# Optimization experiments

Measured on AMD Instinct MI355X. Metric: run time of the kernel, lower is better.

## Reference

```python
import jax, jax.numpy as jnp
import numpy as np

B, S, D, H, DFF = 2, 2048, 1024, 16, 4096
DK = D // H
EPS = 1e-6


def layer_norm(x, alpha, bias):
    # TF reduce_std is biased std; eps added to std (not variance)
    mean = jnp.mean(x, axis=-1, keepdims=True)
    std = jnp.sqrt(jnp.mean((x - mean) ** 2, axis=-1, keepdims=True))
    return alpha * (x - mean) / (std + EPS) + bias


def setup_inputs() -> dict:
    key = jax.random.key(0)
    ks = jax.random.split(key, 10)
    s = 0.02
    return {
        "x": jax.random.normal(ks[0], (B, S, D), jnp.float32),
        "mask": jnp.ones((B, 1, 1, S), jnp.int32),
        "wq": jax.random.normal(ks[1], (D, D), jnp.float32) * s,
        "wk": jax.random.normal(ks[2], (D, D), jnp.float32) * s,
        "wv": jax.random.normal(ks[3], (D, D), jnp.float32) * s,
        "wo": jax.random.normal(ks[4], (D, D), jnp.float32) * s,
        "w1": jax.random.normal(ks[5], (D, DFF), jnp.float32) * s,
        "b1": jnp.zeros((DFF,), jnp.float32),
        "w2": jax.random.normal(ks[6], (DFF, D), jnp.float32) * s,
        "b2": jnp.zeros((D,), jnp.float32),
        "ln1_a": jnp.ones((D,), jnp.float32),
        "ln1_b": jnp.zeros((D,), jnp.float32),
        "ln2_a": jnp.ones((D,), jnp.float32),
        "ln2_b": jnp.zeros((D,), jnp.float32),
    }


def reference(x, mask, wq, wk, wv, wo, w1, b1, w2, b2, ln1_a, ln1_b, ln2_a, ln2_b):
    # --- residual 1: pre-norm self-attention ---
    xn = layer_norm(x, ln1_a, ln1_b)
    q = (xn @ wq).reshape(B, S, H, DK)
    k = (xn @ wk).reshape(B, S, H, DK)
    v = (xn @ wv).reshape(B, S, H, DK)
    scores = jnp.einsum('bqhd,bkhd->bhqk', q, k) / jnp.sqrt(jnp.float32(DK))
    scores = jnp.where(mask == 0, jnp.float32(-1e9), scores)
    attn = jax.nn.softmax(scores, axis=-1)  # dropout = identity at eval
    ctx = jnp.einsum('bhqk,bkhd->bqhd', attn, v).reshape(B, S, D)
    x = x + ctx @ wo
    # --- residual 2: pre-norm FFN ---
    xn = layer_norm(x, ln2_a, ln2_b)
    ff = jax.nn.relu(xn @ w1 + b1) @ w2 + b2
    return x + ff
```

## Files before the change

kernel.cpp:

```cpp
#include <hip/hip_runtime.h>

#define BATCH 2
#define SEQ   2048
#define DMODEL 1024
#define NHEAD 16
#define DHEAD 64
#define DFF_  4096
#define MROWS (BATCH*SEQ)
#define EPS 1e-6f

typedef unsigned short u16;
typedef unsigned int u32;
typedef __bf16 bf16x8 __attribute__((ext_vector_type(8)));
typedef float  f32x4  __attribute__((ext_vector_type(4)));
typedef u32    u32x2  __attribute__((ext_vector_type(2)));

__device__ __forceinline__ float bf2f(u16 h) {
    union { u32 u; float f; } v; v.u = ((u32)h) << 16; return v.f;
}
__device__ __forceinline__ u16 f2bf(float f) {
    union { float f; u32 u; } v; v.f = f;
    u32 u = v.u;
    u32 r = (u + 0x7fffu + ((u >> 16) & 1u)) >> 16;
    return (u16)r;
}

__device__ __forceinline__ void async16(const u16* g, u16* l) {
    __builtin_amdgcn_global_load_lds((const __attribute__((address_space(1))) void*)g,
                                     (__attribute__((address_space(3))) void*)l,
                                     16, 0, 0);
}

__global__ __launch_bounds__(256) void transpose_cvt(const float* __restrict__ in,
                                                     u16* __restrict__ out,
                                                     int R, int C) {
    __shared__ float tile[32][33];
    int c0 = blockIdx.x * 32, r0 = blockIdx.y * 32;
    int x = threadIdx.x, y = threadIdx.y;
    #pragma unroll
    for (int i = 0; i < 32; i += 8)
        tile[y + i][x] = in[(size_t)(r0 + y + i) * C + c0 + x];
    __syncthreads();
    #pragma unroll
    for (int i = 0; i < 32; i += 8)
        out[(size_t)(c0 + y + i) * R + r0 + x] = f2bf(tile[x][y + i]);
}

__global__ __launch_bounds__(256) void transpose_cvt4(const float* __restrict__ i0,
                                                      const float* __restrict__ i1,
                                                      const float* __restrict__ i2,
                                                      const float* __restrict__ i3,
                                                      u16* __restrict__ o0,
                                                      u16* __restrict__ o1,
                                                      u16* __restrict__ o2,
                                                      u16* __restrict__ o3) {
    __shared__ float tile[32][33];
    const float* in; u16* out;
    switch (blockIdx.z) {
        case 0: in = i0; out = o0; break;
        case 1: in = i1; out = o1; break;
        case 2: in = i2; out = o2; break;
        default: in = i3; out = o3; break;
    }
    int c0 = blockIdx.x * 32, r0 = blockIdx.y * 32;
    int x = threadIdx.x, y = threadIdx.y;
    #pragma unroll
    for (int i = 0; i < 32; i += 8)
        tile[y + i][x] = in[(size_t)(r0 + y + i) * DMODEL + c0 + x];
    __syncthreads();
    #pragma unroll
    for (int i = 0; i < 32; i += 8)
        out[(size_t)(c0 + y + i) * DMODEL + r0 + x] = f2bf(tile[x][y + i]);
}

__global__ __launch_bounds__(256) void transpose_v_perm(const u16* __restrict__ qkv,
                                                        u16* __restrict__ vtp) {
    __shared__ u16 tile[64][72];
    int kt = blockIdx.x * 64;
    int bh = blockIdx.y; int b = bh >> 4, h = bh & 15;
    const u16* in = qkv + ((size_t)(b * SEQ + kt)) * 3072 + 2 * DMODEL + h * DHEAD;
    u16* out = vtp + ((size_t)bh * DHEAD) * SEQ;
    int t = threadIdx.x;
    int r = t >> 3, c8 = (t & 7) * 8;
    #pragma unroll
    for (int pass = 0; pass < 2; pass++) {
        int row = r + pass * 32;
        uint4 v = *(const uint4*)(in + (size_t)row * 3072 + c8);
        *(uint4*)&tile[row][c8] = v;
    }
    __syncthreads();
    #pragma unroll
    for (int pass = 0; pass < 2; pass++) {
        int d = r + pass * 32;
        u16 o8[8];
        #pragma unroll
        for (int e = 0; e < 8; e++) {
            int c = c8 + e;
            o8[e] = tile[(c & 3) * 16 + (c >> 2)][d];
        }
        *(uint4*)(out + (size_t)d * SEQ + kt + c8) = *(const uint4*)o8;
    }
}

__global__ __launch_bounds__(256) void ln_kernel(const float* __restrict__ x,
                                                 const float* __restrict__ alpha,
                                                 const float* __restrict__ beta,
                                                 u16* __restrict__ out) {
    int row = blockIdx.x;
    int t = threadIdx.x;
    const float* xr = x + (size_t)row * DMODEL;
    float4 xv = ((const float4*)xr)[t];
    float f0 = xv.x, f1 = xv.y, f2 = xv.z, f3 = xv.w;
    float s1 = f0 + f1 + f2 + f3;
    float s2 = f0*f0 + f1*f1 + f2*f2 + f3*f3;
    #pragma unroll
    for (int off = 32; off >= 1; off >>= 1) {
        s1 += __shfl_xor(s1, off);
        s2 += __shfl_xor(s2, off);
    }
    __shared__ float r1[4], r2[4];
    int w = t >> 6, lane = t & 63;
    if (lane == 0) { r1[w] = s1; r2[w] = s2; }
    __syncthreads();
    s1 = r1[0] + r1[1] + r1[2] + r1[3];
    s2 = r2[0] + r2[1] + r2[2] + r2[3];
    float mean = s1 * (1.0f / DMODEL);
    float var  = s2 * (1.0f / DMODEL) - mean * mean;
    var = fmaxf(var, 0.0f);
    float inv = 1.0f / (sqrtf(var) + EPS);
    float4 av = ((const float4*)alpha)[t];
    float4 bv = ((const float4*)beta)[t];
    ushort4 ov;
    ov.x = f2bf(av.x * (f0 - mean) * inv + bv.x);
    ov.y = f2bf(av.y * (f1 - mean) * inv + bv.y);
    ov.z = f2bf(av.z * (f2 - mean) * inv + bv.z);
    ov.w = f2bf(av.w * (f3 - mean) * inv + bv.w);
    ((ushort4*)(out + (size_t)row * DMODEL))[t] = ov;
}

#define BK 64

template <int AI, int AJ, bool OUT_F32>
__global__ __launch_bounds__(256) void gemm_bt(const u16* __restrict__ A,
                                               const u16* __restrict__ BT,
                                               void* __restrict__ Cp,
                                               const float* __restrict__ bias,
                                               const float* __restrict__ residual,
                                               int M, int N, int K, int do_relu) {
    constexpr int BMt = AI * 32, BNt = AJ * 32;
    __shared__ u16 As[BMt * BK];
    __shared__ u16 Bs[BNt * BK];
    int t = threadIdx.x;
    int bx = blockIdx.x;
    if ((gridDim.x & 7) == 0) {
        int cpx = gridDim.x >> 3;
        bx = (bx & 7) * cpx + (bx >> 3);
    }
    int m0 = blockIdx.y * BMt, n0 = bx * BNt;
    int lane = t & 63, w = t >> 6;
    int wr = w >> 1, wc = w & 1;
    int lhi = lane >> 4, llo = lane & 15;
    int sr = lane >> 3, sk = lane & 7;
    int skx = (sk ^ sr) * 8;

    f32x4 acc[AI][AJ] = {};

    const u16* Ab = A  + (size_t)m0 * K + skx;
    const u16* Bb = BT + (size_t)n0 * K + skx;

    for (int k0 = 0; k0 < K; k0 += BK) {
        __syncthreads();
        #pragma unroll
        for (int j = 0; j < AI; j++) {
            int blk = w * AI + j;
            async16(Ab + (size_t)(blk * 8 + sr) * K + k0, &As[blk * 512]);
        }
        #pragma unroll
        for (int j = 0; j < AJ; j++) {
            int blk = w * AJ + j;
            async16(Bb + (size_t)(blk * 8 + sr) * K + k0, &Bs[blk * 512]);
        }
        __syncthreads();
        #pragma unroll
        for (int kk = 0; kk < 2; kk++) {
            int slot = ((kk * 4 + lhi) ^ (llo & 7)) * 8;
            bf16x8 af[AI], bfr[AJ];
            #pragma unroll
            for (int i = 0; i < AI; i++)
                af[i]  = *(const bf16x8*)(&As[(wr * 16 * AI + i * 16 + llo) * 64 + slot]);
            #pragma unroll
            for (int j = 0; j < AJ; j++)
                bfr[j] = *(const bf16x8*)(&Bs[(wc * 16 * AJ + j * 16 + llo) * 64 + slot]);
            #pragma unroll
            for (int i = 0; i < AI; i++)
                #pragma unroll
                for (int j = 0; j < AJ; j++)
                    acc[i][j] = __builtin_amdgcn_mfma_f32_16x16x32_bf16(af[i], bfr[j], acc[i][j], 0, 0, 0);
        }
    }

    #pragma unroll
    for (int i = 0; i < AI; i++) {
        #pragma unroll
        for (int rr = 0; rr < 4; rr++) {
            int row = m0 + wr * 16 * AI + i * 16 + lhi * 4 + rr;
            #pragma unroll
            for (int j = 0; j < AJ; j++) {
                int col = n0 + wc * 16 * AJ + j * 16 + llo;
                float v = acc[i][j][rr];
                if (bias)      v += bias[col];
                if (residual)  v += residual[(size_t)row * N + col];
                if (do_relu)   v = fmaxf(v, 0.0f);
                size_t idx = (size_t)row * N + col;
                if (OUT_F32) ((float*)Cp)[idx] = v;
                else         ((u16*)Cp)[idx]   = f2bf(v);
            }
        }
    }
}

#define SCL 0.18033688f

__global__ __launch_bounds__(256) void flash_attn(const u16* __restrict__ qkv,
                                                  const u16* __restrict__ vtp,
                                                  const int* __restrict__ mask,
                                                  u16* __restrict__ ctx) {
    __shared__ u16 QPs[64 * 64];
    __shared__ u16 Ks[64 * 64];
    __shared__ u16 VTs[64 * 64];
    __shared__ float mbias[64];

    int t = threadIdx.x;
    int w = t >> 6, lane = t & 63, lhi = lane >> 4, llo = lane & 15;
    int sr = lane >> 3, sk = lane & 7;
    int skx = (sk ^ sr) * 8;

    int f  = (blockIdx.z * NHEAD + blockIdx.y) * (SEQ / 64) + blockIdx.x;
    int s  = f & 31;
    int q0 = (f >> 5) * 64;
    int hb = (s & 7) * 4 + (s >> 3);
    int h = hb & 15, b = hb >> 4;

    const u16* Qg  = qkv + ((size_t)(b * SEQ + q0)) * 3072 + h * DHEAD;
    const u16* Kg  = qkv + ((size_t)(b * SEQ)) * 3072 + DMODEL + h * DHEAD;
    const u16* VTg = vtp + ((size_t)((b * NHEAD + h) * DHEAD)) * SEQ;

    #pragma unroll
    for (int j = 0; j < 2; j++) {
        int blk = w * 2 + j;
        async16(Qg + (size_t)(blk * 8 + sr) * 3072 + skx, &QPs[blk * 512]);
    }
    __syncthreads();
    bf16x8 qf[2];
    #pragma unroll
    for (int kk = 0; kk < 2; kk++)
        qf[kk] = *(const bf16x8*)&QPs[(w * 16 + llo) * 64 + ((kk * 4 + lhi) ^ (llo & 7)) * 8];

    u16* Ps = QPs + w * 1024;

    float l_part[4] = {};
    f32x4 o_acc[4] = {};

    for (int kt = 0; kt < SEQ; kt += 64) {
        __syncthreads();
        #pragma unroll
        for (int j = 0; j < 2; j++) {
            int blk = w * 2 + j;
            async16(Kg  + (size_t)(kt + blk * 8 + sr) * 3072 + skx, &Ks[blk * 512]);
            async16(VTg + (size_t)(blk * 8 + sr) * SEQ + kt + skx,  &VTs[blk * 512]);
        }
        if (t < 64) mbias[t] = (mask[b * SEQ + kt + t] == 0) ? -1.0e12f : 0.0f;
        __syncthreads();

        f32x4 s4[4] = {};
        #pragma unroll
        for (int kk = 0; kk < 2; kk++) {
            #pragma unroll
            for (int j = 0; j < 4; j++) {
                bf16x8 kf = *(const bf16x8*)&Ks[(j * 16 + llo) * 64 +
                                                ((kk * 4 + lhi) ^ (llo & 7)) * 8];
                s4[j] = __builtin_amdgcn_mfma_f32_16x16x32_bf16(qf[kk], kf, s4[j], 0, 0, 0);
            }
        }
        float mb[4];
        #pragma unroll
        for (int j = 0; j < 4; j++) mb[j] = mbias[j * 16 + llo];

        #pragma unroll
        for (int rr = 0; rr < 4; rr++) {
            u32 pu[4];
            #pragma unroll
            for (int j = 0; j < 4; j++) {
                float p = __builtin_amdgcn_exp2f(__builtin_fmaf(s4[j][rr], SCL, mb[j]));
                l_part[rr] += p;
                union { float f; u32 u; } c; c.f = p;
                pu[j] = c.u;
            }
            u32x2 pw;
            pw[0] = (pu[0] >> 16) | (pu[1] & 0xffff0000u);
            pw[1] = (pu[2] >> 16) | (pu[3] & 0xffff0000u);
            int prow = lhi * 4 + rr;
            *(u32x2*)&Ps[prow * 64 + ((llo >> 1) ^ (prow & 7)) * 8 + (llo & 1) * 4] = pw;
        }
        #pragma unroll
        for (int kk = 0; kk < 2; kk++) {
            bf16x8 pf = *(const bf16x8*)&Ps[llo * 64 + ((kk * 4 + lhi) ^ (llo & 7)) * 8];
            #pragma unroll
            for (int nb = 0; nb < 4; nb++) {
                bf16x8 vf = *(const bf16x8*)&VTs[(nb * 16 + llo) * 64 +
                                                 ((kk * 4 + lhi) ^ (llo & 7)) * 8];
                o_acc[nb] = __builtin_amdgcn_mfma_f32_16x16x32_bf16(pf, vf, o_acc[nb], 0, 0, 0);
            }
        }
    }

    #pragma unroll
    for (int rr = 0; rr < 4; rr++) {
        float l = l_part[rr];
        #pragma unroll
        for (int off = 1; off <= 8; off <<= 1) l += __shfl_xor(l, off);
        float inv = __builtin_amdgcn_rcpf(l);
        int row = q0 + w * 16 + lhi * 4 + rr;
        #pragma unroll
        for (int nb = 0; nb < 4; nb++) {
            int col = h * DHEAD + nb * 16 + llo;
            ctx[((size_t)(b * SEQ) + row) * DMODEL + col] = f2bf(o_acc[nb][rr] * inv);
        }
    }
}

extern "C" void kernel_launch(void* const* d_in, const int* in_sizes, int n_in,
                              void* d_out, int out_size, void* d_ws, size_t ws_size,
                              hipStream_t stream) {
    (void)in_sizes; (void)n_in; (void)out_size; (void)ws_size;
    const float* x    = (const float*)d_in[0];
    const int* mask   = (const int*)d_in[1];
    const float* wq   = (const float*)d_in[2];
    const float* wk   = (const float*)d_in[3];
    const float* wv   = (const float*)d_in[4];
    const float* wo   = (const float*)d_in[5];
    const float* w1   = (const float*)d_in[6];
    const float* b1   = (const float*)d_in[7];
    const float* w2   = (const float*)d_in[8];
    const float* b2   = (const float*)d_in[9];
    const float* ln1a = (const float*)d_in[10];
    const float* ln1b = (const float*)d_in[11];
    const float* ln2a = (const float*)d_in[12];
    const float* ln2b = (const float*)d_in[13];
    float* out = (float*)d_out;

    char* wsb = (char*)d_ws;
    const size_t MB = 1024 * 1024;
    u16*   wqkvT = (u16*)(wsb + 0);
    u16*   woT   = (u16*)(wsb + 6 * MB);
    u16*   w1T   = (u16*)(wsb + 8 * MB);
    u16*   w2T   = (u16*)(wsb + 16 * MB);
    u16*   xn    = (u16*)(wsb + 24 * MB);
    float* x2    = (float*)(wsb + 32 * MB);
    u16*   vtp   = (u16*)(wsb + 32 * MB);
    u16*   ctx   = (u16*)(wsb + 48 * MB);
    u16*   qkv   = (u16*)(wsb + 56 * MB);
    u16*   ff1   = (u16*)(wsb + 56 * MB);

    dim3 tb(32, 8);
    transpose_cvt4<<<dim3(DMODEL/32, DMODEL/32, 4), tb, 0, stream>>>(
        wq, wk, wv, wo,
        wqkvT, wqkvT + 1024*1024, wqkvT + 2*1024*1024, woT);
    transpose_cvt<<<dim3(DFF_/32,  DMODEL/32),  tb, 0, stream>>>(w1, w1T, DMODEL, DFF_);
    transpose_cvt<<<dim3(DMODEL/32, DFF_/32),   tb, 0, stream>>>(w2, w2T, DFF_, DMODEL);

    ln_kernel<<<MROWS, 256, 0, stream>>>(x, ln1a, ln1b, xn);
    gemm_bt<4,2,false><<<dim3(3072/64, MROWS/128), 256, 0, stream>>>(xn, wqkvT, qkv,
                                                                     nullptr, nullptr,
                                                                     MROWS, 3072, DMODEL, 0);
    transpose_v_perm<<<dim3(SEQ/64, BATCH*NHEAD), 256, 0, stream>>>(qkv, vtp);
    flash_attn<<<dim3(SEQ/64, NHEAD, BATCH), 256, 0, stream>>>(qkv, vtp, mask, ctx);
    gemm_bt<2,2,true><<<dim3(DMODEL/64, MROWS/64), 256, 0, stream>>>(ctx, woT, x2,
                                                                     nullptr, x,
                                                                     MROWS, DMODEL, DMODEL, 0);
    ln_kernel<<<MROWS, 256, 0, stream>>>(x2, ln2a, ln2b, xn);
    gemm_bt<4,2,false><<<dim3(DFF_/64, MROWS/128), 256, 0, stream>>>(xn, w1T, ff1,
                                                                    b1, nullptr,
                                                                    MROWS, DFF_, DMODEL, 1);
    gemm_bt<2,2,true><<<dim3(DMODEL/64, MROWS/64), 256, 0, stream>>>(ff1, w2T, out,
                                                                    b2, x2,
                                                                    MROWS, DMODEL, DFF_, 0);
}
```

Measured before the change: 372.3 us.

## Split-K the FFN down-projection with atomic accumulation into LN-initialized output

The final FFN down-projection GEMM (K=4096) is split into two K halves along a new grid z dimension, and each half atomically adds its partial into the fp32 output. The second layernorm kernel now pre-initializes the output with residual plus b2, so the GEMM epilogue no longer adds bias or residual. The aim is to double the block count of this long-K GEMM for better CU occupancy. The cost is atomic traffic, an extra full fp32 write in the layernorm, and nondeterministic summation order.

```diff
diff --git a/kernel.cpp b/kernel.cpp
--- a/kernel.cpp
+++ b/kernel.cpp
@@ -105,7 +105,9 @@
 __global__ __launch_bounds__(256) void ln_kernel(const float* __restrict__ x,
                                                  const float* __restrict__ alpha,
                                                  const float* __restrict__ beta,
-                                                 u16* __restrict__ out) {
+                                                 u16* __restrict__ out,
+                                                 const float* __restrict__ abias,
+                                                 float* __restrict__ finit) {
     int row = blockIdx.x;
     int t = threadIdx.x;
     const float* xr = x + (size_t)row * DMODEL;
@@ -136,11 +138,17 @@
     ov.z = f2bf(av.z * (f2 - mean) * inv + bv.z);
     ov.w = f2bf(av.w * (f3 - mean) * inv + bv.w);
     ((ushort4*)(out + (size_t)row * DMODEL))[t] = ov;
+    if (finit) {
+        float4 bb = ((const float4*)abias)[t];
+        float4 iv;
+        iv.x = f0 + bb.x; iv.y = f1 + bb.y; iv.z = f2 + bb.z; iv.w = f3 + bb.w;
+        ((float4*)(finit + (size_t)row * DMODEL))[t] = iv;
+    }
 }
 
 #define BK 64
 
-template <int AI, int AJ, bool OUT_F32>
+template <int AI, int AJ, bool OUT_F32, bool ATOMIC = false>
 __global__ __launch_bounds__(256) void gemm_bt(const u16* __restrict__ A,
                                                const u16* __restrict__ BT,
                                                void* __restrict__ Cp,
@@ -163,12 +171,15 @@
     int sr = lane >> 3, sk = lane & 7;
     int skx = (sk ^ sr) * 8;
 
+    int Ksub = K / (int)gridDim.z;
+    int kbeg = (int)blockIdx.z * Ksub, kend = kbeg + Ksub;
+
     f32x4 acc[AI][AJ] = {};
 
     const u16* Ab = A  + (size_t)m0 * K + skx;
     const u16* Bb = BT + (size_t)n0 * K + skx;
 
-    for (int k0 = 0; k0 < K; k0 += BK) {
+    for (int k0 = kbeg; k0 < kend; k0 += BK) {
         __syncthreads();
         #pragma unroll
         for (int j = 0; j < AI; j++) {
@@ -212,8 +223,12 @@
                 if (residual)  v += residual[(size_t)row * N + col];
                 if (do_relu)   v = fmaxf(v, 0.0f);
                 size_t idx = (size_t)row * N + col;
-                if (OUT_F32) ((float*)Cp)[idx] = v;
-                else         ((u16*)Cp)[idx]   = f2bf(v);
+                if (OUT_F32) {
+                    if (ATOMIC) atomicAdd(&((float*)Cp)[idx], v);
+                    else        ((float*)Cp)[idx] = v;
+                } else {
+                    ((u16*)Cp)[idx] = f2bf(v);
+                }
             }
         }
     }
@@ -369,7 +384,7 @@
     transpose_cvt<<<dim3(DFF_/32,  DMODEL/32),  tb, 0, stream>>>(w1, w1T, DMODEL, DFF_);
     transpose_cvt<<<dim3(DMODEL/32, DFF_/32),   tb, 0, stream>>>(w2, w2T, DFF_, DMODEL);
 
-    ln_kernel<<<MROWS, 256, 0, stream>>>(x, ln1a, ln1b, xn);
+    ln_kernel<<<MROWS, 256, 0, stream>>>(x, ln1a, ln1b, xn, nullptr, nullptr);
     gemm_bt<4,2,false><<<dim3(3072/64, MROWS/128), 256, 0, stream>>>(xn, wqkvT, qkv,
                                                                      nullptr, nullptr,
                                                                      MROWS, 3072, DMODEL, 0);
@@ -378,11 +393,10 @@
     gemm_bt<2,2,true><<<dim3(DMODEL/64, MROWS/64), 256, 0, stream>>>(ctx, woT, x2,
                                                                      nullptr, x,
                                                                      MROWS, DMODEL, DMODEL, 0);
-    ln_kernel<<<MROWS, 256, 0, stream>>>(x2, ln2a, ln2b, xn);
+    ln_kernel<<<MROWS, 256, 0, stream>>>(x2, ln2a, ln2b, xn, b2, out);
     gemm_bt<4,2,false><<<dim3(DFF_/64, MROWS/128), 256, 0, stream>>>(xn, w1T, ff1,
                                                                     b1, nullptr,
                                                                     MROWS, DFF_, DMODEL, 1);
-    gemm_bt<2,2,true><<<dim3(DMODEL/64, MROWS/64), 256, 0, stream>>>(ff1, w2T, out,
-                                                                    b2, x2,
-                                                                    MROWS, DMODEL, DFF_, 0);
-}
+    gemm_bt<2,2,true,true><<<dim3(DMODEL/64, MROWS/64, 2), 256, 0, stream>>>(
+        ff1, w2T, out, nullptr, nullptr, MROWS, DMODEL, DFF_, 0);
+}
```

Result: slower. 383.9 us (+3.1%).
